# Performance work log

Hardware: AMD Instinct MI355X
Metric: run time of the kernel (lower is better)

Reference implementation:

```python
import jax, jax.numpy as jnp
import numpy as np

B, S, H, F, E, TOPK = 2, 2048, 1024, 4096, 8, 2


def setup_inputs() -> dict:
    key = jax.random.key(0)
    k0, k1, k2, k3, k4 = jax.random.split(key, 5)
    scale = 0.02
    return {
        "hidden_states": jax.random.normal(k0, (B, S, H), dtype=jnp.float32),
        "gate_w": jax.random.normal(k1, (E, H), dtype=jnp.float32) * scale,
        "w1": jax.random.normal(k2, (E, F, H), dtype=jnp.float32) * scale,
        "w2": jax.random.normal(k3, (E, H, F), dtype=jnp.float32) * scale,
        "w3": jax.random.normal(k4, (E, F, H), dtype=jnp.float32) * scale,
        "top_k": TOPK,
    }


def reference(hidden_states, gate_w, w1, w2, w3, top_k):
    b, s, h = hidden_states.shape
    num_experts = gate_w.shape[0]
    x = hidden_states.reshape(-1, h)                      # [T,H]
    router_logits = x @ gate_w.T                          # [T,E]
    routing = jax.nn.softmax(router_logits.astype(jnp.float32), axis=-1)
    top_w, top_e = jax.lax.top_k(routing, top_k)          # [T,K]
    top_w = top_w / top_w.sum(axis=-1, keepdims=True)     # renormalize over top-k
    top_w = top_w.astype(x.dtype)
    # combine weights [T,E]: zero for unselected experts (faithful to masked dispatch)
    cw = (jax.nn.one_hot(top_e, num_experts, dtype=x.dtype) * top_w[..., None]).sum(axis=1)
    out = jnp.zeros_like(x)
    for e in range(num_experts):  # fixed, small expert count
        inter = jax.nn.silu(x @ w1[e].T) * (x @ w3[e].T)  # [T,F]
        out = out + cw[:, e:e + 1] * (inter @ w2[e].T)
    return out.reshape(b, s, h), router_logits
```

## Files before the change

### kernel.cpp

```cpp
#include <hip/hip_runtime.h>
#include <stdint.h>

#define T 4096
#define HDIM 1024
#define FDIM 4096
#define NE 8
#define MAXROWS 10240

typedef __bf16 bf16x8 __attribute__((ext_vector_type(8)));
typedef float f32x4 __attribute__((ext_vector_type(4)));

__device__ __forceinline__ unsigned short f2bf(float f) {
    unsigned u = __builtin_bit_cast(unsigned, f);
    u += 0x7FFFu + ((u >> 16) & 1u);
    return (unsigned short)(u >> 16);
}

__device__ __forceinline__ void cp16(const void* g, const void* lds) {
    __builtin_amdgcn_global_load_lds(
        (const __attribute__((address_space(1))) unsigned int*)g,
        (__attribute__((address_space(3))) unsigned int*)(unsigned int)(unsigned long long)lds,
        16, 0, 0);
}

__global__ void conv_x_k(const float* __restrict__ x, unsigned short* __restrict__ xb) {
    size_t i = ((size_t)blockIdx.x * 256 + threadIdx.x) * 8;
    float4 a = *(const float4*)(x + i);
    float4 b = *(const float4*)(x + i + 4);
    uint4 v;
    v.x = (unsigned)f2bf(a.x) | ((unsigned)f2bf(a.y) << 16);
    v.y = (unsigned)f2bf(a.z) | ((unsigned)f2bf(a.w) << 16);
    v.z = (unsigned)f2bf(b.x) | ((unsigned)f2bf(b.y) << 16);
    v.w = (unsigned)f2bf(b.z) | ((unsigned)f2bf(b.w) << 16);
    *(uint4*)(xb + i) = v;
}

__global__ void conv_all_k(const float* __restrict__ w1, const float* __restrict__ w3,
                           const float* __restrict__ w2,
                           unsigned short* __restrict__ wb1, unsigned short* __restrict__ wb3,
                           unsigned short* __restrict__ wb2) {
    int z = blockIdx.y;
    const float* s = (z == 0) ? w1 : (z == 1) ? w3 : w2;
    unsigned short* d = (z == 0) ? wb1 : (z == 1) ? wb3 : wb2;
    size_t i = ((size_t)blockIdx.x * 256 + threadIdx.x) * 8;
    float4 a = *(const float4*)(s + i);
    float4 b = *(const float4*)(s + i + 4);
    uint4 v;
    v.x = (unsigned)f2bf(a.x) | ((unsigned)f2bf(a.y) << 16);
    v.y = (unsigned)f2bf(a.z) | ((unsigned)f2bf(a.w) << 16);
    v.z = (unsigned)f2bf(b.x) | ((unsigned)f2bf(b.y) << 16);
    v.w = (unsigned)f2bf(b.z) | ((unsigned)f2bf(b.w) << 16);
    *(uint4*)(d + i) = v;
}

__global__ void conv_w13_k(const float* __restrict__ src, unsigned short* __restrict__ dst,
                           int f0, int Fc) {
    int e = blockIdx.y;
    size_t rem = ((size_t)blockIdx.x * 256 + threadIdx.x) * 8;
    const float* s = src + ((size_t)e * FDIM + f0) * HDIM + rem;
    unsigned short* d = dst + (size_t)e * Fc * HDIM + rem;
    float4 a = *(const float4*)(s);
    float4 b = *(const float4*)(s + 4);
    uint4 v;
    v.x = (unsigned)f2bf(a.x) | ((unsigned)f2bf(a.y) << 16);
    v.y = (unsigned)f2bf(a.z) | ((unsigned)f2bf(a.w) << 16);
    v.z = (unsigned)f2bf(b.x) | ((unsigned)f2bf(b.y) << 16);
    v.w = (unsigned)f2bf(b.z) | ((unsigned)f2bf(b.w) << 16);
    *(uint4*)(d) = v;
}

__global__ void conv_w2_k(const float* __restrict__ src, unsigned short* __restrict__ dst,
                          int f0, int Fc, int fcShift) {
    int e = blockIdx.y;
    size_t idx = ((size_t)blockIdx.x * 256 + threadIdx.x) * 8;
    int h = (int)(idx >> fcShift);
    int c = (int)(idx & (size_t)(Fc - 1));
    const float* s = src + ((size_t)e * HDIM + h) * FDIM + f0 + c;
    unsigned short* d = dst + (size_t)e * HDIM * Fc + idx;
    float4 a = *(const float4*)(s);
    float4 b = *(const float4*)(s + 4);
    uint4 v;
    v.x = (unsigned)f2bf(a.x) | ((unsigned)f2bf(a.y) << 16);
    v.y = (unsigned)f2bf(a.z) | ((unsigned)f2bf(a.w) << 16);
    v.z = (unsigned)f2bf(b.x) | ((unsigned)f2bf(b.y) << 16);
    v.w = (unsigned)f2bf(b.z) | ((unsigned)f2bf(b.w) << 16);
    *(uint4*)(d) = v;
}

__global__ void router_k(const float* __restrict__ x, const float* __restrict__ gw,
                         float* __restrict__ logits_out, int* __restrict__ cnt,
                         int* __restrict__ list, float* __restrict__ wlist) {
    int w = threadIdx.x >> 6, lane = threadIdx.x & 63;
    int t = blockIdx.x * 4 + w;
    float acc[NE];
#pragma unroll
    for (int e = 0; e < NE; ++e) acc[e] = 0.f;
    for (int i = 0; i < HDIM / 64; ++i) {
        int h = i * 64 + lane;
        float xv = x[(size_t)t * HDIM + h];
#pragma unroll
        for (int e = 0; e < NE; ++e) acc[e] += xv * gw[e * HDIM + h];
    }
#pragma unroll
    for (int e = 0; e < NE; ++e)
#pragma unroll
        for (int off = 32; off; off >>= 1) acc[e] += __shfl_xor(acc[e], off);
    if (lane == 0) {
#pragma unroll
        for (int e = 0; e < NE; ++e) logits_out[(size_t)t * NE + e] = acc[e];
        int e1 = 0;
#pragma unroll
        for (int e = 1; e < NE; ++e) if (acc[e] > acc[e1]) e1 = e;
        int e2 = (e1 == 0) ? 1 : 0;
#pragma unroll
        for (int e = 0; e < NE; ++e) { if (e == e1) continue; if (acc[e] > acc[e2]) e2 = e; }
        float wa = 1.f / (1.f + expf(acc[e2] - acc[e1]));
        float wb = 1.f - wa;
        int p1 = atomicAdd(&cnt[e1], 1); list[e1 * T + p1] = t; wlist[e1 * T + p1] = wa;
        int p2 = atomicAdd(&cnt[e2], 1); list[e2 * T + p2] = t; wlist[e2 * T + p2] = wb;
    }
}

__global__ void offsets_k(const int* __restrict__ cnt, int* __restrict__ poff) {
    if (threadIdx.x == 0) {
        int o = 0; poff[0] = 0;
        for (int e = 0; e < NE; ++e) { o += ((cnt[e] + 255) >> 8) << 8; poff[e + 1] = o; }
    }
}

__global__ void compact_k(const int* __restrict__ cnt, const int* __restrict__ poff,
                          const int* __restrict__ list, const float* __restrict__ wlist,
                          int* __restrict__ tok_row, float* __restrict__ w_row) {
    int gid = blockIdx.x * 256 + threadIdx.x;
    int e = gid >> 12, i = gid & (T - 1);
    int pc = poff[e + 1] - poff[e];
    if (i < pc) {
        int row = poff[e] + i;
        if (i < cnt[e]) { tok_row[row] = list[e * T + i]; w_row[row] = wlist[e * T + i]; }
        else           { tok_row[row] = T;               w_row[row] = 0.f; }
    }
}

__global__ __launch_bounds__(512, 2) void gemm1_k(
    const unsigned short* __restrict__ xb, const unsigned short* __restrict__ wb1,
    const unsigned short* __restrict__ wb3, const int* __restrict__ tok_row,
    const int* __restrict__ poff, unsigned short* __restrict__ inter, int Fc) {

    __shared__ __align__(16) unsigned short lds[2 * 32768];
    __shared__ int toks[256];
    __shared__ int e_sh;

    int row0 = blockIdx.y * 256;
    if (row0 >= poff[NE]) return;
    int tid = threadIdx.x;
    if (tid == 0) { int e = 0; while (row0 >= poff[e + 1]) ++e; e_sh = e; }
    if (tid < 256) toks[tid] = tok_row[row0 + tid];
    __syncthreads();
    int e = e_sh;
    int fr0 = blockIdx.x * 128;
    const unsigned short* w1p = wb1 + ((size_t)e * Fc + fr0) * HDIM;
    const unsigned short* w3p = wb3 + ((size_t)e * Fc + fr0) * HDIM;

    int wv = tid >> 6, lane = tid & 63;
    int quad = lane >> 4, l16 = lane & 15;
    int wm = (wv >> 1) * 64;
    int wn = (wv & 1) * 64;

    int sr = lane >> 3;
    int sc = (lane & 7) ^ sr;
    unsigned a_off[4];
#pragma unroll
    for (int jj = 0; jj < 4; ++jj)
        a_off[jj] = (unsigned)toks[(wv * 4 + jj) * 8 + sr] * HDIM + sc * 8;
    const unsigned short* b1b = w1p + (size_t)(wv * 16 + sr) * HDIM + sc * 8;
    const unsigned short* b3b = w3p + (size_t)(wv * 16 + sr) * HDIM + sc * 8;

    char* ldsc = (char*)lds;
    unsigned dstA  = (unsigned)(wv * 4) * 1024u;
    unsigned dstB1 = 32768u + (unsigned)(wv * 2) * 1024u;
    unsigned dstB3 = 49152u + (unsigned)(wv * 2) * 1024u;

    f32x4 acc1[4][4], acc3[4][4];
#pragma unroll
    for (int a = 0; a < 4; ++a)
#pragma unroll
        for (int b = 0; b < 4; ++b) {
            acc1[a][b] = f32x4{0.f, 0.f, 0.f, 0.f};
            acc3[a][b] = f32x4{0.f, 0.f, 0.f, 0.f};
        }

#pragma unroll
    for (int jj = 0; jj < 4; ++jj)
        cp16(xb + a_off[jj], ldsc + dstA + jj * 1024);
#pragma unroll
    for (int jj = 0; jj < 2; ++jj) {
        cp16(b1b + (size_t)jj * 8 * HDIM, ldsc + dstB1 + jj * 1024);
        cp16(b3b + (size_t)jj * 8 * HDIM, ldsc + dstB3 + jj * 1024);
    }
    __syncthreads();

#pragma unroll 1
    for (int k = 0; k < 16; ++k) {
        const unsigned short* sb = lds + (k & 1) * 32768;

        if (k < 15) {
            char* db = ldsc + ((k + 1) & 1) * 65536;
            int ko = (k + 1) * 64;
#pragma unroll
            for (int jj = 0; jj < 4; ++jj)
                cp16(xb + a_off[jj] + ko, db + dstA + jj * 1024);
#pragma unroll
            for (int jj = 0; jj < 2; ++jj) {
                cp16(b1b + (size_t)jj * 8 * HDIM + ko, db + dstB1 + jj * 1024);
                cp16(b3b + (size_t)jj * 8 * HDIM + ko, db + dstB3 + jj * 1024);
            }
        }

#pragma unroll
        for (int ks = 0; ks < 2; ++ks) {
            int cb0 = ks * 4 + quad;
            bf16x8 af[4], b1f[4], b3f[4];
#pragma unroll
            for (int mi = 0; mi < 4; ++mi) {
                int m = wm + mi * 16 + l16;
                af[mi] = *(const bf16x8*)(sb + m * 64 + ((cb0 ^ (m & 7)) * 8));
            }
#pragma unroll
            for (int ni = 0; ni < 4; ++ni) {
                int n = wn + ni * 16 + l16;
                int sw = (cb0 ^ (n & 7)) * 8;
                b1f[ni] = *(const bf16x8*)(sb + 16384 + n * 64 + sw);
                b3f[ni] = *(const bf16x8*)(sb + 24576 + n * 64 + sw);
            }
            __builtin_amdgcn_s_setprio(1);
#pragma unroll
            for (int ni = 0; ni < 4; ++ni)
#pragma unroll
                for (int mi = 0; mi < 4; ++mi) {
                    acc1[mi][ni] = __builtin_amdgcn_mfma_f32_16x16x32_bf16(af[mi], b1f[ni], acc1[mi][ni], 0, 0, 0);
                    acc3[mi][ni] = __builtin_amdgcn_mfma_f32_16x16x32_bf16(af[mi], b3f[ni], acc3[mi][ni], 0, 0, 0);
                }
            __builtin_amdgcn_s_setprio(0);
        }
        __syncthreads();
    }

#pragma unroll
    for (int mi = 0; mi < 4; ++mi)
#pragma unroll
        for (int ni = 0; ni < 4; ++ni)
#pragma unroll
            for (int r = 0; r < 4; ++r) {
                int m = wm + mi * 16 + quad * 4 + r;
                int n = wn + ni * 16 + l16;
                float v1 = acc1[mi][ni][r], v3 = acc3[mi][ni][r];
                float hval = (v1 / (1.f + __expf(-v1))) * v3;
                inter[(size_t)(row0 + m) * Fc + fr0 + n] = f2bf(hval);
            }
}

__global__ __launch_bounds__(256, 3) void gemm2_k(
    const unsigned short* __restrict__ inter, const unsigned short* __restrict__ wb2,
    const int* __restrict__ tok_row, const float* __restrict__ w_row,
    const int* __restrict__ poff, float* __restrict__ out, int Fc) {

    __shared__ __align__(16) unsigned short As[128 * 64];
    __shared__ __align__(16) unsigned short Bs[128 * 64];
    __shared__ int e_sh;

    int row0 = blockIdx.y * 128;
    if (row0 >= poff[NE]) return;
    int tid = threadIdx.x;
    if (tid == 0) { int e = 0; while (row0 >= poff[e + 1]) ++e; e_sh = e; }
    __syncthreads();
    int e = e_sh;
    int n0 = blockIdx.x * 128;

    int wv = tid >> 6, lane = tid & 63;
    int quad = lane >> 4, l16 = lane & 15;
    int wm = (wv >> 1) * 64, wn = (wv & 1) * 64;

    int sr = lane >> 3;
    int sc = (lane & 7) ^ sr;
    const unsigned short* a_b = inter + (size_t)(row0 + wv * 32 + sr) * Fc + sc * 8;
    const unsigned short* b_b = wb2 + ((size_t)e * HDIM + n0 + wv * 32 + sr) * Fc + sc * 8;

    f32x4 acc[4][4];
#pragma unroll
    for (int a = 0; a < 4; ++a)
#pragma unroll
        for (int b = 0; b < 4; ++b) acc[a][b] = f32x4{0.f, 0.f, 0.f, 0.f};

    for (int k0 = 0; k0 < Fc; k0 += 64) {
#pragma unroll
        for (int jj = 0; jj < 4; ++jj) {
            int j = wv * 4 + jj;
            cp16(a_b + (size_t)jj * 8 * Fc + k0, As + j * 512);
            cp16(b_b + (size_t)jj * 8 * Fc + k0, Bs + j * 512);
        }
        __syncthreads();
#pragma unroll
        for (int ks = 0; ks < 2; ++ks) {
            int cb0 = ks * 4 + quad;
            bf16x8 af[4];
#pragma unroll
            for (int mi = 0; mi < 4; ++mi) {
                int m = wm + mi * 16 + l16;
                af[mi] = *(const bf16x8*)(As + m * 64 + ((cb0 ^ (m & 7)) * 8));
            }
#pragma unroll
            for (int ni = 0; ni < 4; ++ni) {
                int n = wn + ni * 16 + l16;
                bf16x8 bf = *(const bf16x8*)(Bs + n * 64 + ((cb0 ^ (n & 7)) * 8));
#pragma unroll
                for (int mi = 0; mi < 4; ++mi)
                    acc[mi][ni] = __builtin_amdgcn_mfma_f32_16x16x32_bf16(af[mi], bf, acc[mi][ni], 0, 0, 0);
            }
        }
        __syncthreads();
    }
#pragma unroll
    for (int mi = 0; mi < 4; ++mi)
#pragma unroll
        for (int r = 0; r < 4; ++r) {
            int m = wm + mi * 16 + quad * 4 + r;
            int grow = row0 + m;
            float wr = w_row[grow];
            if (wr != 0.f) {
                int t = tok_row[grow];
                float* op = out + (size_t)t * HDIM + n0;
#pragma unroll
                for (int ni = 0; ni < 4; ++ni)
                    atomicAdd(op + wn + ni * 16 + l16, wr * acc[mi][ni][r]);
            }
        }
}

extern "C" void kernel_launch(void* const* d_in, const int* in_sizes, int n_in,
                              void* d_out, int out_size, void* d_ws, size_t ws_size,
                              hipStream_t stream) {
    const float* x  = (const float*)d_in[0];
    const float* gw = (const float*)d_in[1];
    const float* w1 = (const float*)d_in[2];
    const float* w2 = (const float*)d_in[3];
    const float* w3 = (const float*)d_in[4];
    float* out = (float*)d_out;
    float* logits = out + (size_t)T * HDIM;

    char* ws = (char*)d_ws;
    size_t off = 0;
    auto alloc = [&](size_t b) {
        off = (off + 255) & ~(size_t)255;
        void* p = ws + off;
        off += b;
        return p;
    };
    int* cnt        = (int*)alloc(NE * 4);
    int* poff       = (int*)alloc((NE + 1) * 4);
    int* list       = (int*)alloc((size_t)NE * T * 4);
    float* wlist    = (float*)alloc((size_t)NE * T * 4);
    int* tok_row    = (int*)alloc(MAXROWS * 4);
    float* w_row    = (float*)alloc(MAXROWS * 4);
    unsigned short* xb = (unsigned short*)alloc((size_t)(T + 1) * HDIM * 2);
    size_t fixed_off = off;

    int Fc = 4096, fcShift = 12;
    for (;;) {
        size_t need = fixed_off + 3 * ((size_t)NE * Fc * HDIM * 2) + (size_t)MAXROWS * Fc * 2 + 1024;
        if (need <= ws_size || Fc == 512) break;
        Fc >>= 1; fcShift -= 1;
    }
    unsigned short* wb1 = (unsigned short*)alloc((size_t)NE * Fc * HDIM * 2);
    unsigned short* wb3 = (unsigned short*)alloc((size_t)NE * Fc * HDIM * 2);
    unsigned short* wb2 = (unsigned short*)alloc((size_t)NE * HDIM * Fc * 2);
    unsigned short* inter = (unsigned short*)alloc((size_t)MAXROWS * Fc * 2);

    hipMemsetAsync(cnt, 0, NE * 4, stream);
    hipMemsetAsync(out, 0, (size_t)T * HDIM * 4, stream);
    hipMemsetAsync(xb + (size_t)T * HDIM, 0, HDIM * 2, stream);
    conv_x_k<<<(T * HDIM / 8) / 256, 256, 0, stream>>>(x, xb);
    router_k<<<T / 4, 256, 0, stream>>>(x, gw, logits, cnt, list, wlist);
    offsets_k<<<1, 64, 0, stream>>>(cnt, poff);
    compact_k<<<NE * T / 256, 256, 0, stream>>>(cnt, poff, list, wlist, tok_row, w_row);

    int nMT1 = MAXROWS / 256;
    int nMT2 = MAXROWS / 128;
    if (Fc == FDIM) {
        conv_all_k<<<dim3((size_t)NE * FDIM * HDIM / 8 / 256, 3), 256, 0, stream>>>(
            w1, w3, w2, wb1, wb3, wb2);
        gemm1_k<<<dim3(FDIM / 128, nMT1), 512, 0, stream>>>(xb, wb1, wb3, tok_row, poff, inter, FDIM);
        gemm2_k<<<dim3(HDIM / 128, nMT2), 256, 0, stream>>>(inter, wb2, tok_row, w_row, poff, out, FDIM);
    } else {
        for (int f0 = 0; f0 < FDIM; f0 += Fc) {
            conv_w13_k<<<dim3(Fc / 2, NE), 256, 0, stream>>>(w1, wb1, f0, Fc);
            conv_w13_k<<<dim3(Fc / 2, NE), 256, 0, stream>>>(w3, wb3, f0, Fc);
            conv_w2_k<<<dim3(HDIM * Fc / 2048, NE), 256, 0, stream>>>(w2, wb2, f0, Fc, fcShift);
            gemm1_k<<<dim3(Fc / 128, nMT1), 512, 0, stream>>>(xb, wb1, wb3, tok_row, poff, inter, Fc);
            gemm2_k<<<dim3(HDIM / 128, nMT2), 256, 0, stream>>>(inter, wb2, tok_row, w_row, poff, out, Fc);
        }
    }
}
```

Baseline: 790.7 us.

## Split gemm1 main loop into four phases with interleaved prefetch and fine-grained waits

Restructures the gate/up GEMM main loop into four sub-phases (w1/w3 for each half of the K tile). Each phase reads LDS fragments, issues part of the next tile's global-to-LDS copies, then runs its MFMAs, guarded by s_waitcnt vmcnt and raw s_barrier instead of a single full __syncthreads per iteration. The last iteration is peeled. The intent is to spread memory issue across compute and cut barrier stalls. The cost is more barriers per iteration and fragile manual waitcnt ordering that could race if the counts are wrong.

```diff
diff --git a/kernel.cpp b/kernel.cpp
--- a/kernel.cpp
+++ b/kernel.cpp
@@ -192,34 +192,75 @@
 #pragma unroll
     for (int jj = 0; jj < 4; ++jj)
         cp16(xb + a_off[jj], ldsc + dstA + jj * 1024);
-#pragma unroll
-    for (int jj = 0; jj < 2; ++jj) {
-        cp16(b1b + (size_t)jj * 8 * HDIM, ldsc + dstB1 + jj * 1024);
-        cp16(b3b + (size_t)jj * 8 * HDIM, ldsc + dstB3 + jj * 1024);
-    }
-    __syncthreads();
+    cp16(b1b,                      ldsc + dstB1);
+    cp16(b1b + (size_t)8 * HDIM,   ldsc + dstB1 + 1024);
+    cp16(b3b,                      ldsc + dstB3);
+    cp16(b3b + (size_t)8 * HDIM,   ldsc + dstB3 + 1024);
+
+    bf16x8 af[4];
 
 #pragma unroll 1
-    for (int k = 0; k < 16; ++k) {
+    for (int k = 0; k < 15; ++k) {
         const unsigned short* sb = lds + (k & 1) * 32768;
-
-        if (k < 15) {
-            char* db = ldsc + ((k + 1) & 1) * 65536;
-            int ko = (k + 1) * 64;
-#pragma unroll
-            for (int jj = 0; jj < 4; ++jj)
-                cp16(xb + a_off[jj] + ko, db + dstA + jj * 1024);
-#pragma unroll
-            for (int jj = 0; jj < 2; ++jj) {
-                cp16(b1b + (size_t)jj * 8 * HDIM + ko, db + dstB1 + jj * 1024);
-                cp16(b3b + (size_t)jj * 8 * HDIM + ko, db + dstB3 + jj * 1024);
-            }
-        }
-
-#pragma unroll
-        for (int ks = 0; ks < 2; ++ks) {
-            int cb0 = ks * 4 + quad;
-            bf16x8 af[4], b1f[4], b3f[4];
+        char* db = ldsc + ((k + 1) & 1) * 65536;
+        int ko = (k + 1) * 64;
+
+        asm volatile("s_waitcnt vmcnt(2)" ::: "memory");
+        __builtin_amdgcn_s_barrier();
+        __builtin_amdgcn_sched_barrier(0);
+        {
+            bf16x8 b1f[4];
+#pragma unroll
+            for (int mi = 0; mi < 4; ++mi) {
+                int m = wm + mi * 16 + l16;
+                af[mi] = *(const bf16x8*)(sb + m * 64 + ((quad ^ (m & 7)) * 8));
+            }
+#pragma unroll
+            for (int ni = 0; ni < 4; ++ni) {
+                int n = wn + ni * 16 + l16;
+                b1f[ni] = *(const bf16x8*)(sb + 16384 + n * 64 + ((quad ^ (n & 7)) * 8));
+            }
+            cp16(xb + a_off[0] + ko, db + dstA);
+            cp16(xb + a_off[1] + ko, db + dstA + 1024);
+            asm volatile("s_waitcnt lgkmcnt(0)" ::: "memory");
+            __builtin_amdgcn_sched_barrier(0);
+            __builtin_amdgcn_s_setprio(1);
+#pragma unroll
+            for (int ni = 0; ni < 4; ++ni)
+#pragma unroll
+                for (int mi = 0; mi < 4; ++mi)
+                    acc1[mi][ni] = __builtin_amdgcn_mfma_f32_16x16x32_bf16(af[mi], b1f[ni], acc1[mi][ni], 0, 0, 0);
+            __builtin_amdgcn_s_setprio(0);
+        }
+
+        asm volatile("s_waitcnt vmcnt(2)" ::: "memory");
+        __builtin_amdgcn_s_barrier();
+        __builtin_amdgcn_sched_barrier(0);
+        {
+            bf16x8 b3f[4];
+#pragma unroll
+            for (int ni = 0; ni < 4; ++ni) {
+                int n = wn + ni * 16 + l16;
+                b3f[ni] = *(const bf16x8*)(sb + 24576 + n * 64 + ((quad ^ (n & 7)) * 8));
+            }
+            cp16(xb + a_off[2] + ko, db + dstA + 2048);
+            cp16(xb + a_off[3] + ko, db + dstA + 3072);
+            asm volatile("s_waitcnt lgkmcnt(0)" ::: "memory");
+            __builtin_amdgcn_sched_barrier(0);
+            __builtin_amdgcn_s_setprio(1);
+#pragma unroll
+            for (int ni = 0; ni < 4; ++ni)
+#pragma unroll
+                for (int mi = 0; mi < 4; ++mi)
+                    acc3[mi][ni] = __builtin_amdgcn_mfma_f32_16x16x32_bf16(af[mi], b3f[ni], acc3[mi][ni], 0, 0, 0);
+            __builtin_amdgcn_s_setprio(0);
+        }
+
+        __builtin_amdgcn_s_barrier();
+        __builtin_amdgcn_sched_barrier(0);
+        {
+            bf16x8 b1f[4];
+            int cb0 = 4 + quad;
 #pragma unroll
             for (int mi = 0; mi < 4; ++mi) {
                 int m = wm + mi * 16 + l16;
@@ -228,21 +269,133 @@
 #pragma unroll
             for (int ni = 0; ni < 4; ++ni) {
                 int n = wn + ni * 16 + l16;
-                int sw = (cb0 ^ (n & 7)) * 8;
-                b1f[ni] = *(const bf16x8*)(sb + 16384 + n * 64 + sw);
-                b3f[ni] = *(const bf16x8*)(sb + 24576 + n * 64 + sw);
-            }
+                b1f[ni] = *(const bf16x8*)(sb + 16384 + n * 64 + ((cb0 ^ (n & 7)) * 8));
+            }
+            cp16(b1b + ko,                    db + dstB1);
+            cp16(b1b + (size_t)8 * HDIM + ko, db + dstB1 + 1024);
+            asm volatile("s_waitcnt lgkmcnt(0)" ::: "memory");
+            __builtin_amdgcn_sched_barrier(0);
             __builtin_amdgcn_s_setprio(1);
 #pragma unroll
             for (int ni = 0; ni < 4; ++ni)
 #pragma unroll
-                for (int mi = 0; mi < 4; ++mi) {
+                for (int mi = 0; mi < 4; ++mi)
                     acc1[mi][ni] = __builtin_amdgcn_mfma_f32_16x16x32_bf16(af[mi], b1f[ni], acc1[mi][ni], 0, 0, 0);
+            __builtin_amdgcn_s_setprio(0);
+        }
+
+        __builtin_amdgcn_s_barrier();
+        __builtin_amdgcn_sched_barrier(0);
+        {
+            bf16x8 b3f[4];
+            int cb0 = 4 + quad;
+#pragma unroll
+            for (int ni = 0; ni < 4; ++ni) {
+                int n = wn + ni * 16 + l16;
+                b3f[ni] = *(const bf16x8*)(sb + 24576 + n * 64 + ((cb0 ^ (n & 7)) * 8));
+            }
+            cp16(b3b + ko,                    db + dstB3);
+            cp16(b3b + (size_t)8 * HDIM + ko, db + dstB3 + 1024);
+            asm volatile("s_waitcnt lgkmcnt(0)" ::: "memory");
+            __builtin_amdgcn_sched_barrier(0);
+            __builtin_amdgcn_s_setprio(1);
+#pragma unroll
+            for (int ni = 0; ni < 4; ++ni)
+#pragma unroll
+                for (int mi = 0; mi < 4; ++mi)
                     acc3[mi][ni] = __builtin_amdgcn_mfma_f32_16x16x32_bf16(af[mi], b3f[ni], acc3[mi][ni], 0, 0, 0);
-                }
             __builtin_amdgcn_s_setprio(0);
         }
-        __syncthreads();
+    }
+
+    {
+        const unsigned short* sb = lds + 32768;
+
+        asm volatile("s_waitcnt vmcnt(2)" ::: "memory");
+        __builtin_amdgcn_s_barrier();
+        __builtin_amdgcn_sched_barrier(0);
+        {
+            bf16x8 b1f[4];
+#pragma unroll
+            for (int mi = 0; mi < 4; ++mi) {
+                int m = wm + mi * 16 + l16;
+                af[mi] = *(const bf16x8*)(sb + m * 64 + ((quad ^ (m & 7)) * 8));
+            }
+#pragma unroll
+            for (int ni = 0; ni < 4; ++ni) {
+                int n = wn + ni * 16 + l16;
+                b1f[ni] = *(const bf16x8*)(sb + 16384 + n * 64 + ((quad ^ (n & 7)) * 8));
+            }
+            asm volatile("s_waitcnt lgkmcnt(0)" ::: "memory");
+            __builtin_amdgcn_sched_barrier(0);
+#pragma unroll
+            for (int ni = 0; ni < 4; ++ni)
+#pragma unroll
+                for (int mi = 0; mi < 4; ++mi)
+                    acc1[mi][ni] = __builtin_amdgcn_mfma_f32_16x16x32_bf16(af[mi], b1f[ni], acc1[mi][ni], 0, 0, 0);
+        }
+
+        asm volatile("s_waitcnt vmcnt(0)" ::: "memory");
+        __builtin_amdgcn_s_barrier();
+        __builtin_amdgcn_sched_barrier(0);
+        {
+            bf16x8 b3f[4];
+#pragma unroll
+            for (int ni = 0; ni < 4; ++ni) {
+                int n = wn + ni * 16 + l16;
+                b3f[ni] = *(const bf16x8*)(sb + 24576 + n * 64 + ((quad ^ (n & 7)) * 8));
+            }
+            asm volatile("s_waitcnt lgkmcnt(0)" ::: "memory");
+            __builtin_amdgcn_sched_barrier(0);
+#pragma unroll
+            for (int ni = 0; ni < 4; ++ni)
+#pragma unroll
+                for (int mi = 0; mi < 4; ++mi)
+                    acc3[mi][ni] = __builtin_amdgcn_mfma_f32_16x16x32_bf16(af[mi], b3f[ni], acc3[mi][ni], 0, 0, 0);
+        }
+
+        __builtin_amdgcn_s_barrier();
+        __builtin_amdgcn_sched_barrier(0);
+        {
+            bf16x8 b1f[4];
+            int cb0 = 4 + quad;
+#pragma unroll
+            for (int mi = 0; mi < 4; ++mi) {
+                int m = wm + mi * 16 + l16;
+                af[mi] = *(const bf16x8*)(sb + m * 64 + ((cb0 ^ (m & 7)) * 8));
+            }
+#pragma unroll
+            for (int ni = 0; ni < 4; ++ni) {
+                int n = wn + ni * 16 + l16;
+                b1f[ni] = *(const bf16x8*)(sb + 16384 + n * 64 + ((cb0 ^ (n & 7)) * 8));
+            }
+            asm volatile("s_waitcnt lgkmcnt(0)" ::: "memory");
+            __builtin_amdgcn_sched_barrier(0);
+#pragma unroll
+            for (int ni = 0; ni < 4; ++ni)
+#pragma unroll
+                for (int mi = 0; mi < 4; ++mi)
+                    acc1[mi][ni] = __builtin_amdgcn_mfma_f32_16x16x32_bf16(af[mi], b1f[ni], acc1[mi][ni], 0, 0, 0);
+        }
+
+        __builtin_amdgcn_s_barrier();
+        __builtin_amdgcn_sched_barrier(0);
+        {
+            bf16x8 b3f[4];
+            int cb0 = 4 + quad;
+#pragma unroll
+            for (int ni = 0; ni < 4; ++ni) {
+                int n = wn + ni * 16 + l16;
+                b3f[ni] = *(const bf16x8*)(sb + 24576 + n * 64 + ((cb0 ^ (n & 7)) * 8));
+            }
+            asm volatile("s_waitcnt lgkmcnt(0)" ::: "memory");
+            __builtin_amdgcn_sched_barrier(0);
+#pragma unroll
+            for (int ni = 0; ni < 4; ++ni)
+#pragma unroll
+                for (int mi = 0; mi < 4; ++mi)
+                    acc3[mi][ni] = __builtin_amdgcn_mfma_f32_16x16x32_bf16(af[mi], b3f[ni], acc3[mi][ni], 0, 0, 0);
+        }
     }
 
 #pragma unroll
```

After: 786.2 us. No clear change (-0.6%).

## Double-buffer gemm2 LDS loads, swizzle GEMM block order, batch router atomics

Applied to the files above, without the earlier changes.

gemm2 now keeps two LDS stages and issues the next K-tile's global-to-LDS copies before computing on the current one. This overlaps memory latency with MFMA work, and occupancy is lowered to 2 blocks to fit the doubled shared memory. Both GEMMs remap block indices into 8x8 groups so neighbouring blocks share weight and activation tiles in L2. The router now handles 64 tokens per 1024-thread block and aggregates its counters in shared memory, issuing one global atomic per expert per block. The gemm2 loop count is hardcoded to 64 iterations, which is only correct when Fc equals 4096.

```diff
diff --git a/kernel.cpp b/kernel.cpp
--- a/kernel.cpp
+++ b/kernel.cpp
@@ -87,37 +87,62 @@
     *(uint4*)(d) = v;
 }
 
-__global__ void router_k(const float* __restrict__ x, const float* __restrict__ gw,
-                         float* __restrict__ logits_out, int* __restrict__ cnt,
-                         int* __restrict__ list, float* __restrict__ wlist) {
-    int w = threadIdx.x >> 6, lane = threadIdx.x & 63;
-    int t = blockIdx.x * 4 + w;
-    float acc[NE];
-#pragma unroll
-    for (int e = 0; e < NE; ++e) acc[e] = 0.f;
-    for (int i = 0; i < HDIM / 64; ++i) {
-        int h = i * 64 + lane;
-        float xv = x[(size_t)t * HDIM + h];
-#pragma unroll
-        for (int e = 0; e < NE; ++e) acc[e] += xv * gw[e * HDIM + h];
-    }
-#pragma unroll
-    for (int e = 0; e < NE; ++e)
-#pragma unroll
-        for (int off = 32; off; off >>= 1) acc[e] += __shfl_xor(acc[e], off);
-    if (lane == 0) {
-#pragma unroll
-        for (int e = 0; e < NE; ++e) logits_out[(size_t)t * NE + e] = acc[e];
-        int e1 = 0;
-#pragma unroll
-        for (int e = 1; e < NE; ++e) if (acc[e] > acc[e1]) e1 = e;
-        int e2 = (e1 == 0) ? 1 : 0;
-#pragma unroll
-        for (int e = 0; e < NE; ++e) { if (e == e1) continue; if (acc[e] > acc[e2]) e2 = e; }
-        float wa = 1.f / (1.f + expf(acc[e2] - acc[e1]));
-        float wb = 1.f - wa;
-        int p1 = atomicAdd(&cnt[e1], 1); list[e1 * T + p1] = t; wlist[e1 * T + p1] = wa;
-        int p2 = atomicAdd(&cnt[e2], 1); list[e2 * T + p2] = t; wlist[e2 * T + p2] = wb;
+__global__ __launch_bounds__(1024) void router_k(
+    const float* __restrict__ x, const float* __restrict__ gw,
+    float* __restrict__ logits_out, int* __restrict__ cnt,
+    int* __restrict__ list, float* __restrict__ wlist) {
+    __shared__ int   ltok[128];
+    __shared__ int   lexp[128];
+    __shared__ float lww[128];
+    __shared__ int   lpos[128];
+    __shared__ int   bcnt[NE];
+    __shared__ int   bbase[NE];
+
+    int tid = threadIdx.x, wave = tid >> 6, lane = tid & 63;
+    if (tid < NE) bcnt[tid] = 0;
+
+#pragma unroll 1
+    for (int j = 0; j < 4; ++j) {
+        int t = blockIdx.x * 64 + wave * 4 + j;
+        float acc[NE];
+#pragma unroll
+        for (int e = 0; e < NE; ++e) acc[e] = 0.f;
+        for (int i = 0; i < HDIM / 64; ++i) {
+            int h = i * 64 + lane;
+            float xv = x[(size_t)t * HDIM + h];
+#pragma unroll
+            for (int e = 0; e < NE; ++e) acc[e] += xv * gw[e * HDIM + h];
+        }
+#pragma unroll
+        for (int e = 0; e < NE; ++e)
+#pragma unroll
+            for (int off = 32; off; off >>= 1) acc[e] += __shfl_xor(acc[e], off);
+        if (lane == 0) {
+#pragma unroll
+            for (int e = 0; e < NE; ++e) logits_out[(size_t)t * NE + e] = acc[e];
+            int e1 = 0;
+#pragma unroll
+            for (int e = 1; e < NE; ++e) if (acc[e] > acc[e1]) e1 = e;
+            int e2 = (e1 == 0) ? 1 : 0;
+#pragma unroll
+            for (int e = 0; e < NE; ++e) { if (e == e1) continue; if (acc[e] > acc[e2]) e2 = e; }
+            float wa = 1.f / (1.f + expf(acc[e2] - acc[e1]));
+            float wb = 1.f - wa;
+            int s = (wave * 4 + j) * 2;
+            ltok[s] = t;     lexp[s] = e1;     lww[s] = wa;
+            ltok[s + 1] = t; lexp[s + 1] = e2; lww[s + 1] = wb;
+        }
+    }
+    __syncthreads();
+    if (tid < 128) lpos[tid] = atomicAdd(&bcnt[lexp[tid]], 1);
+    __syncthreads();
+    if (tid < NE) bbase[tid] = atomicAdd(&cnt[tid], bcnt[tid]);
+    __syncthreads();
+    if (tid < 128) {
+        int e = lexp[tid];
+        int p = bbase[e] + lpos[tid];
+        list[e * T + p] = ltok[tid];
+        wlist[e * T + p] = lww[tid];
     }
 }
 
@@ -150,14 +175,18 @@
     __shared__ int toks[256];
     __shared__ int e_sh;
 
-    int row0 = blockIdx.y * 256;
+    int bx = blockIdx.x, by = blockIdx.y;
+    int Xf = (bx >> 3) * 8 + (by & 7);
+    int Ys = (by >> 3) * 8 + (bx & 7);
+
+    int row0 = Ys * 256;
     if (row0 >= poff[NE]) return;
     int tid = threadIdx.x;
     if (tid == 0) { int e = 0; while (row0 >= poff[e + 1]) ++e; e_sh = e; }
     if (tid < 256) toks[tid] = tok_row[row0 + tid];
     __syncthreads();
     int e = e_sh;
-    int fr0 = blockIdx.x * 128;
+    int fr0 = Xf * 128;
     const unsigned short* w1p = wb1 + ((size_t)e * Fc + fr0) * HDIM;
     const unsigned short* w3p = wb3 + ((size_t)e * Fc + fr0) * HDIM;
 
@@ -259,22 +288,25 @@
             }
 }
 
-__global__ __launch_bounds__(256, 3) void gemm2_k(
+__global__ __launch_bounds__(256, 2) void gemm2_k(
     const unsigned short* __restrict__ inter, const unsigned short* __restrict__ wb2,
     const int* __restrict__ tok_row, const float* __restrict__ w_row,
     const int* __restrict__ poff, float* __restrict__ out, int Fc) {
 
-    __shared__ __align__(16) unsigned short As[128 * 64];
-    __shared__ __align__(16) unsigned short Bs[128 * 64];
+    __shared__ __align__(16) unsigned short lds[2 * 16384];
     __shared__ int e_sh;
 
-    int row0 = blockIdx.y * 128;
+    int bx = blockIdx.x, by = blockIdx.y;
+    int Xn = by & 7;
+    int Ys = (by >> 3) * 8 + bx;
+
+    int row0 = Ys * 128;
     if (row0 >= poff[NE]) return;
     int tid = threadIdx.x;
     if (tid == 0) { int e = 0; while (row0 >= poff[e + 1]) ++e; e_sh = e; }
     __syncthreads();
     int e = e_sh;
-    int n0 = blockIdx.x * 128;
+    int n0 = Xn * 128;
 
     int wv = tid >> 6, lane = tid & 63;
     int quad = lane >> 4, l16 = lane & 15;
@@ -285,20 +317,37 @@
     const unsigned short* a_b = inter + (size_t)(row0 + wv * 32 + sr) * Fc + sc * 8;
     const unsigned short* b_b = wb2 + ((size_t)e * HDIM + n0 + wv * 32 + sr) * Fc + sc * 8;
 
+    char* ldsc = (char*)lds;
+
     f32x4 acc[4][4];
 #pragma unroll
     for (int a = 0; a < 4; ++a)
 #pragma unroll
         for (int b = 0; b < 4; ++b) acc[a][b] = f32x4{0.f, 0.f, 0.f, 0.f};
 
-    for (int k0 = 0; k0 < Fc; k0 += 64) {
-#pragma unroll
-        for (int jj = 0; jj < 4; ++jj) {
-            int j = wv * 4 + jj;
-            cp16(a_b + (size_t)jj * 8 * Fc + k0, As + j * 512);
-            cp16(b_b + (size_t)jj * 8 * Fc + k0, Bs + j * 512);
-        }
-        __syncthreads();
+#pragma unroll
+    for (int jj = 0; jj < 4; ++jj) {
+        int j = wv * 4 + jj;
+        cp16(a_b + (size_t)jj * 8 * Fc, ldsc + j * 1024);
+        cp16(b_b + (size_t)jj * 8 * Fc, ldsc + 16384 + j * 1024);
+    }
+    __syncthreads();
+
+#pragma unroll 1
+    for (int k = 0; k < 64; ++k) {
+        const unsigned short* sb = lds + (k & 1) * 16384;
+
+        if (k < 63) {
+            char* db = ldsc + ((k + 1) & 1) * 32768;
+            int ko = (k + 1) * 64;
+#pragma unroll
+            for (int jj = 0; jj < 4; ++jj) {
+                int j = wv * 4 + jj;
+                cp16(a_b + (size_t)jj * 8 * Fc + ko, db + j * 1024);
+                cp16(b_b + (size_t)jj * 8 * Fc + ko, db + 16384 + j * 1024);
+            }
+        }
+
 #pragma unroll
         for (int ks = 0; ks < 2; ++ks) {
             int cb0 = ks * 4 + quad;
@@ -306,12 +355,12 @@
 #pragma unroll
             for (int mi = 0; mi < 4; ++mi) {
                 int m = wm + mi * 16 + l16;
-                af[mi] = *(const bf16x8*)(As + m * 64 + ((cb0 ^ (m & 7)) * 8));
+                af[mi] = *(const bf16x8*)(sb + m * 64 + ((cb0 ^ (m & 7)) * 8));
             }
 #pragma unroll
             for (int ni = 0; ni < 4; ++ni) {
                 int n = wn + ni * 16 + l16;
-                bf16x8 bf = *(const bf16x8*)(Bs + n * 64 + ((cb0 ^ (n & 7)) * 8));
+                bf16x8 bf = *(const bf16x8*)(sb + 8192 + n * 64 + ((cb0 ^ (n & 7)) * 8));
 #pragma unroll
                 for (int mi = 0; mi < 4; ++mi)
                     acc[mi][ni] = __builtin_amdgcn_mfma_f32_16x16x32_bf16(af[mi], bf, acc[mi][ni], 0, 0, 0);
@@ -319,6 +368,7 @@
         }
         __syncthreads();
     }
+
 #pragma unroll
     for (int mi = 0; mi < 4; ++mi)
 #pragma unroll
@@ -379,7 +429,7 @@
     hipMemsetAsync(out, 0, (size_t)T * HDIM * 4, stream);
     hipMemsetAsync(xb + (size_t)T * HDIM, 0, HDIM * 2, stream);
     conv_x_k<<<(T * HDIM / 8) / 256, 256, 0, stream>>>(x, xb);
-    router_k<<<T / 4, 256, 0, stream>>>(x, gw, logits, cnt, list, wlist);
+    router_k<<<T / 64, 1024, 0, stream>>>(x, gw, logits, cnt, list, wlist);
     offsets_k<<<1, 64, 0, stream>>>(cnt, poff);
     compact_k<<<NE * T / 256, 256, 0, stream>>>(cnt, poff, list, wlist, tok_row, w_row);
 
```

Measured after the change: 781.2 us. No clear change (-1.2%).
